# Optimization experiments

Measured on AMD Instinct MI355X. Metric: run time of the kernel, lower is better.

Reference implementation:

```python
import jax, jax.numpy as jnp
import numpy as np

B, V, C = 4, 50000, 160


def rotation_6d_to_matrix(d6):
    """pytorch3d-style 6D rotation -> 3x3 matrix (rows b1,b2,b3)."""
    a1, a2 = d6[..., :3], d6[..., 3:]
    eps = 1e-8
    b1 = a1 / jnp.maximum(jnp.linalg.norm(a1, axis=-1, keepdims=True), eps)
    a2p = a2 - jnp.sum(b1 * a2, axis=-1, keepdims=True) * b1
    b2 = a2p / jnp.maximum(jnp.linalg.norm(a2p, axis=-1, keepdims=True), eps)
    b3 = jnp.cross(b1, b2)
    return jnp.stack([b1, b2, b3], axis=-2)  # (..., 3, 3)


def setup_inputs() -> dict:
    key = jax.random.key(0)
    k1, k2, k3, k4, k5 = jax.random.split(key, 5)
    X = jax.random.normal(k1, (B, V, 3), dtype=jnp.float32)
    V_nodes = jax.random.normal(k2, (B, C, 3), dtype=jnp.float32) * 0.1
    rot6d_nodes = jax.random.normal(k3, (B, C, 6), dtype=jnp.float32)
    W_nodes = jax.random.uniform(k4, (V, C), dtype=jnp.float32)
    W_nodes = W_nodes / jnp.sum(W_nodes, axis=1, keepdims=True)  # row-normalized skinning weights
    idx_nn_to_nodes = jax.random.randint(k5, (C,), 0, V, dtype=jnp.int64)
    return {"X": X, "V_nodes": V_nodes, "rot6d_nodes": rot6d_nodes,
            "W_nodes": W_nodes, "idx_nn_to_nodes": idx_nn_to_nodes}


def reference(X, V_nodes, rot6d_nodes, W_nodes, idx_nn_to_nodes):
    # R: (B, C, 3, 3)
    R = rotation_6d_to_matrix(rot6d_nodes)
    # gather node centers: (B, C, 3)
    center = X[:, idx_nn_to_nodes, :]
    # disp: (B, V, C, 3)
    disp = X[:, :, None, :] - center[:, None, :, :]
    # rotate displacement by per-node rotation, add back center + node offset
    Rdisp = jnp.einsum('bvcd,bckd->bvck', disp, R) \
            + center[:, None, :, :] + V_nodes[:, None, :, :]  # (B, V, C, 3)
    # weighted skinning sum over nodes: (B, V, 3)
    out = jnp.einsum('vc,bvck->bvk', W_nodes, Rdisp)
    return out
```

## Files before the change

### kernel.cpp

```cpp
#include <hip/hip_runtime.h>

#define Bv 4
#define Vv 50000
#define Cv 160

__global__ void precompute_A(const float* __restrict__ X,
                             const float* __restrict__ Vn,
                             const float* __restrict__ r6,
                             const int* __restrict__ idx,
                             float* __restrict__ A) {
    int i = blockIdx.x * blockDim.x + threadIdx.x;
    if (i >= Bv * Cv) return;
    int b = i / Cv, c = i % Cv;

    const float* d6 = r6 + (size_t)(b * Cv + c) * 6;
    float a1x = d6[0], a1y = d6[1], a1z = d6[2];
    float a2x = d6[3], a2y = d6[4], a2z = d6[5];

    float n1 = fmaxf(sqrtf(a1x*a1x + a1y*a1y + a1z*a1z), 1e-8f);
    float b1x = a1x / n1, b1y = a1y / n1, b1z = a1z / n1;

    float d = b1x*a2x + b1y*a2y + b1z*a2z;
    float px = a2x - d*b1x, py = a2y - d*b1y, pz = a2z - d*b1z;
    float n2 = fmaxf(sqrtf(px*px + py*py + pz*pz), 1e-8f);
    float b2x = px / n2, b2y = py / n2, b2z = pz / n2;

    float b3x = b1y*b2z - b1z*b2y;
    float b3y = b1z*b2x - b1x*b2z;
    float b3z = b1x*b2y - b1y*b2x;

    int iv = idx[c];
    const float* xc = X + ((size_t)b * Vv + iv) * 3;
    float cx = xc[0], cy = xc[1], cz = xc[2];
    const float* vn = Vn + (size_t)(b * Cv + c) * 3;
    float vx = vn[0], vy = vn[1], vz = vn[2];

    float* Ao = A + (size_t)(b * Cv + c) * 12;
    Ao[0] = b1x; Ao[1] = b1y; Ao[2] = b1z;
    Ao[3] = b2x; Ao[4] = b2y; Ao[5] = b2z;
    Ao[6] = b3x; Ao[7] = b3y; Ao[8] = b3z;
    Ao[9]  = cx + vx - (b1x*cx + b1y*cy + b1z*cz);
    Ao[10] = cy + vy - (b2x*cx + b2y*cy + b2z*cz);
    Ao[11] = cz + vz - (b3x*cx + b3y*cy + b3z*cz);
}

__global__ __launch_bounds__(256) void deform_main(const float* __restrict__ X,
                                                   const float* __restrict__ W,
                                                   const float* __restrict__ A,
                                                   float* __restrict__ out) {
    const int tid  = threadIdx.x;
    const int lane = tid & 63;
    const int b    = __builtin_amdgcn_readfirstlane(tid >> 6);
    const int v0   = blockIdx.x * 64;
    const int v    = v0 + lane;
    const bool valid = (v < Vv);
    const int vc   = valid ? v : (Vv - 1);

    const float4* __restrict__ Wrow = (const float4*)(W + (size_t)vc * Cv);
    const float4* __restrict__ A4   = (const float4*)(A + (size_t)b * Cv * 12);

    const float* xp = X + ((size_t)b * Vv + vc) * 3;
    float x0 = xp[0], x1 = xp[1], x2 = xp[2];

    float acc[12];
#pragma unroll
    for (int j = 0; j < 12; ++j) acc[j] = 0.0f;

#pragma unroll 2
    for (int c4 = 0; c4 < Cv / 4; ++c4) {
        float4 wq = Wrow[c4];
        const float wj[4] = {wq.x, wq.y, wq.z, wq.w};
#pragma unroll
        for (int j = 0; j < 4; ++j) {
            int c = c4 * 4 + j;
            float4 a0 = A4[c * 3 + 0];
            float4 a1 = A4[c * 3 + 1];
            float4 a2 = A4[c * 3 + 2];
            float w = wj[j];
            acc[0]  = fmaf(w, a0.x, acc[0]);
            acc[1]  = fmaf(w, a0.y, acc[1]);
            acc[2]  = fmaf(w, a0.z, acc[2]);
            acc[3]  = fmaf(w, a0.w, acc[3]);
            acc[4]  = fmaf(w, a1.x, acc[4]);
            acc[5]  = fmaf(w, a1.y, acc[5]);
            acc[6]  = fmaf(w, a1.z, acc[6]);
            acc[7]  = fmaf(w, a1.w, acc[7]);
            acc[8]  = fmaf(w, a2.x, acc[8]);
            acc[9]  = fmaf(w, a2.y, acc[9]);
            acc[10] = fmaf(w, a2.z, acc[10]);
            acc[11] = fmaf(w, a2.w, acc[11]);
        }
    }

    if (valid) {
        float o0 = acc[0]*x0 + acc[1]*x1 + acc[2]*x2  + acc[9];
        float o1 = acc[3]*x0 + acc[4]*x1 + acc[5]*x2  + acc[10];
        float o2 = acc[6]*x0 + acc[7]*x1 + acc[8]*x2  + acc[11];
        float* op = out + ((size_t)b * Vv + v) * 3;
        op[0] = o0; op[1] = o1; op[2] = o2;
    }
}

extern "C" void kernel_launch(void* const* d_in, const int* in_sizes, int n_in,
                              void* d_out, int out_size, void* d_ws, size_t ws_size,
                              hipStream_t stream) {
    const float* X   = (const float*)d_in[0];
    const float* Vn  = (const float*)d_in[1];
    const float* r6  = (const float*)d_in[2];
    const float* W   = (const float*)d_in[3];
    const int*   idx = (const int*)d_in[4];
    float* out = (float*)d_out;
    float* A = (float*)d_ws;

    precompute_A<<<(Bv * Cv + 255) / 256, 256, 0, stream>>>(X, Vn, r6, idx, A);
    deform_main<<<(Vv + 63) / 64, 256, 0, stream>>>(X, W, A, out);
}
```

Measured before the change: 101.2 us.

## Split node reduction across two wave halves with shared-memory combine

```diff
diff --git a/kernel.cpp b/kernel.cpp
--- a/kernel.cpp
+++ b/kernel.cpp
@@ -44,60 +44,64 @@
     Ao[11] = cz + vz - (b3x*cx + b3y*cy + b3z*cz);
 }
 
-__global__ __launch_bounds__(256) void deform_main(const float* __restrict__ X,
+__global__ __launch_bounds__(512) void deform_main(const float* __restrict__ X,
                                                    const float* __restrict__ W,
                                                    const float* __restrict__ A,
                                                    float* __restrict__ out) {
+    __shared__ float P[4 * 64 * 13];
+
     const int tid  = threadIdx.x;
     const int lane = tid & 63;
-    const int b    = __builtin_amdgcn_readfirstlane(tid >> 6);
+    const int wv   = __builtin_amdgcn_readfirstlane(tid >> 6);
+    const int b    = wv & 3;
+    const int half = wv >> 2;
     const int v0   = blockIdx.x * 64;
     const int v    = v0 + lane;
     const bool valid = (v < Vv);
     const int vc   = valid ? v : (Vv - 1);
 
-    const float4* __restrict__ Wrow = (const float4*)(W + (size_t)vc * Cv);
-    const float4* __restrict__ A4   = (const float4*)(A + (size_t)b * Cv * 12);
-
-    const float* xp = X + ((size_t)b * Vv + vc) * 3;
-    float x0 = xp[0], x1 = xp[1], x2 = xp[2];
+    const float4* __restrict__ Wrow =
+        (const float4*)(W + (size_t)vc * Cv) + half * 20;
+    const float* __restrict__ Ab = A + ((size_t)b * Cv + (size_t)half * 80) * 12;
 
     float acc[12];
 #pragma unroll
     for (int j = 0; j < 12; ++j) acc[j] = 0.0f;
 
 #pragma unroll 2
-    for (int c4 = 0; c4 < Cv / 4; ++c4) {
+    for (int c4 = 0; c4 < 20; ++c4) {
         float4 wq = Wrow[c4];
         const float wj[4] = {wq.x, wq.y, wq.z, wq.w};
 #pragma unroll
         for (int j = 0; j < 4; ++j) {
-            int c = c4 * 4 + j;
-            float4 a0 = A4[c * 3 + 0];
-            float4 a1 = A4[c * 3 + 1];
-            float4 a2 = A4[c * 3 + 2];
+            const float* a = Ab + (size_t)(c4 * 4 + j) * 12;
             float w = wj[j];
-            acc[0]  = fmaf(w, a0.x, acc[0]);
-            acc[1]  = fmaf(w, a0.y, acc[1]);
-            acc[2]  = fmaf(w, a0.z, acc[2]);
-            acc[3]  = fmaf(w, a0.w, acc[3]);
-            acc[4]  = fmaf(w, a1.x, acc[4]);
-            acc[5]  = fmaf(w, a1.y, acc[5]);
-            acc[6]  = fmaf(w, a1.z, acc[6]);
-            acc[7]  = fmaf(w, a1.w, acc[7]);
-            acc[8]  = fmaf(w, a2.x, acc[8]);
-            acc[9]  = fmaf(w, a2.y, acc[9]);
-            acc[10] = fmaf(w, a2.z, acc[10]);
-            acc[11] = fmaf(w, a2.w, acc[11]);
+#pragma unroll
+            for (int k = 0; k < 12; ++k) acc[k] = fmaf(w, a[k], acc[k]);
         }
     }
 
-    if (valid) {
-        float o0 = acc[0]*x0 + acc[1]*x1 + acc[2]*x2  + acc[9];
-        float o1 = acc[3]*x0 + acc[4]*x1 + acc[5]*x2  + acc[10];
-        float o2 = acc[6]*x0 + acc[7]*x1 + acc[8]*x2  + acc[11];
-        float* op = out + ((size_t)b * Vv + v) * 3;
-        op[0] = o0; op[1] = o1; op[2] = o2;
+    if (half) {
+        float* p = &P[(b * 64 + lane) * 13];
+#pragma unroll
+        for (int j = 0; j < 12; ++j) p[j] = acc[j];
+    }
+    __syncthreads();
+
+    if (!half) {
+        const float* p = &P[(b * 64 + lane) * 13];
+#pragma unroll
+        for (int j = 0; j < 12; ++j) acc[j] += p[j];
+
+        if (valid) {
+            const float* xp = X + ((size_t)b * Vv + v) * 3;
+            float x0 = xp[0], x1 = xp[1], x2 = xp[2];
+            float o0 = acc[0]*x0 + acc[1]*x1 + acc[2]*x2 + acc[9];
+            float o1 = acc[3]*x0 + acc[4]*x1 + acc[5]*x2 + acc[10];
+            float o2 = acc[6]*x0 + acc[7]*x1 + acc[8]*x2 + acc[11];
+            float* op = out + ((size_t)b * Vv + v) * 3;
+            op[0] = o0; op[1] = o1; op[2] = o2;
+        }
     }
 }
 
@@ -113,5 +117,5 @@
     float* A = (float*)d_ws;
 
     precompute_A<<<(Bv * Cv + 255) / 256, 256, 0, stream>>>(X, Vn, r6, idx, A);
-    deform_main<<<(Vv + 63) / 64, 256, 0, stream>>>(X, W, A, out);
+    deform_main<<<(Vv + 63) / 64, 512, 0, stream>>>(X, W, A, out);
 }
```

After: 100.1 us. No clear change (-1.0%).
